# Performance work log

Hardware: AMD Instinct MI355X
Metric: run time of the kernel (lower is better)

## Reference

```python
import jax, jax.numpy as jnp
import numpy as np

N_NODES = 50000
N_EDGES = 800000
DIM = 64
N_REL = 16
N_Q = 8192
FEAT = 4
N_LAYERS = 2


def setup_inputs() -> dict:
    key = jax.random.key(0)
    ks = jax.random.split(key, 16)
    s = 0.1
    return {
        "node_feat": jax.random.normal(ks[0], (N_NODES, FEAT), jnp.float32),
        "edge_index": jax.random.randint(ks[1], (2, N_EDGES), 0, N_NODES),
        "edge_type": jax.random.randint(ks[2], (N_EDGES,), 0, N_REL),
        "heads": jax.random.randint(ks[3], (N_Q,), 0, N_NODES),
        "rels": jax.random.randint(ks[4], (N_Q,), 0, N_REL),
        "tails": jax.random.randint(ks[5], (N_Q,), 0, N_NODES),
        # parameters (stored as [in, out] so y = x @ W + b)
        "in_w": jax.random.normal(ks[6], (FEAT, DIM), jnp.float32) * s,
        "in_b": jnp.zeros((DIM,), jnp.float32),
        "rel_w": jax.random.normal(ks[7], (N_LAYERS, N_REL, DIM, DIM), jnp.float32) * s,
        "self_w": jax.random.normal(ks[8], (N_LAYERS, DIM, DIM), jnp.float32) * s,
        "self_b": jnp.zeros((N_LAYERS, DIM), jnp.float32),
        "rel_emb": jax.random.normal(ks[9], (N_REL, DIM), jnp.float32) * s,
        "sc_w1": jax.random.normal(ks[10], (3 * DIM, DIM), jnp.float32) * s,
        "sc_b1": jnp.zeros((DIM,), jnp.float32),
        "sc_w2": jax.random.normal(ks[11], (DIM, 1), jnp.float32) * s,
        "sc_b2": jnp.zeros((1,), jnp.float32),
    }


def reference(node_feat, edge_index, edge_type, heads, rels, tails,
              in_w, in_b, rel_w, self_w, self_b, rel_emb,
              sc_w1, sc_b1, sc_w2, sc_b2):
    N = node_feat.shape[0]
    src, dst = edge_index[0], edge_index[1]
    # encoder input projection
    x = jax.nn.relu(node_feat @ in_w + in_b)  # [N, D]
    # degree normalization (same deg for every layer)
    deg = jax.ops.segment_sum(jnp.ones_like(dst, dtype=x.dtype), dst, num_segments=N)
    deg = jnp.maximum(deg, 1.0)[:, None]  # [N, 1]
    L = rel_w.shape[0]
    for l in range(L):
        out = x @ self_w[l] + self_b[l]  # self-loop, [N, D]
        # per-relation transform of every node, then per-edge gather by (src, rel)
        # equals the torch per-relation masked gather->matmul->scatter_add
        xw = jnp.einsum('nd,rdo->nro', x, rel_w[l])  # [N, R, D]
        msg = xw[src, edge_type]                     # [E, D]
        agg = jax.ops.segment_sum(msg, dst, num_segments=N)  # [N, D]
        x = jax.nn.relu(out + agg / deg)
    # scoring
    z_h = x[heads]
    z_t = x[tails]
    r = rel_emb[rels]
    c = jnp.concatenate([z_h, z_t, r], axis=-1)  # [Q, 3D]
    h = jax.nn.relu(c @ sc_w1 + sc_b1)
    return (h @ sc_w2 + sc_b2)[:, 0]  # [Q]
```

## Files before the change

kernel.cpp:

```cpp
#include <hip/hip_runtime.h>
#include <hip/hip_bf16.h>
#include <cstdint>
#include <cstddef>

#define N_NODES 50000
#define N_EDGES 800000
#define DIM 64
#define N_REL 16
#define N_Q 8192
#define NKEY (N_NODES * 16)
#define KDIM 1088
#define SROW 1096
#define TILE 16
#define NKB 34
#define WTL (4 * NKB * 512)
#define NBKT 196

#define NB_PROJ 12500
#define NB_WPREP 544
#define NB_BINA 196
#define NB_W1P 48
#define NB_REB 4

typedef __attribute__((ext_vector_type(8))) short bf16x8;
typedef __attribute__((ext_vector_type(4))) float f32x4;

__device__ __forceinline__ unsigned short f2bf(float f) {
    unsigned int b = __float_as_uint(f);
    return (unsigned short)((b + 0x7FFFu + ((b >> 16) & 1u)) >> 16);
}
__device__ __forceinline__ float bf2f(unsigned short u) {
    return __uint_as_float(((unsigned int)u) << 16);
}

__global__ __launch_bounds__(256) void k_prep(
    const float* __restrict__ nf, const float* __restrict__ inw,
    const float* __restrict__ inb, unsigned short* __restrict__ xbf,
    const float* __restrict__ rel_w, const float* __restrict__ self_w,
    unsigned short* __restrict__ wt, const int* __restrict__ dst,
    int* __restrict__ btot, const float* __restrict__ sc_w1,
    unsigned short* __restrict__ w1p, const float* __restrict__ rel_emb,
    unsigned short* __restrict__ reb)
{
    __shared__ int h[NBKT];
    const int b = blockIdx.x, tid = threadIdx.x;
    if (b < NB_PROJ) {
        int t = b * 256 + tid;
        int n = t >> 6, o = t & 63;
        float4 f = *reinterpret_cast<const float4*>(nf + (size_t)n * 4);
        float a = inb[o] + f.x * inw[o] + f.y * inw[64 + o] + f.z * inw[128 + o] + f.w * inw[192 + o];
        xbf[t] = f2bf(a > 0.f ? a : 0.f);
    } else if (b < NB_PROJ + NB_WPREP) {
        int i = (b - NB_PROJ) * 256 + tid;
        int j = i & 7;
        int lane = (i >> 3) & 63;
        int rest = i >> 9;
        int t = rest % NKB;
        int gl = rest / NKB;
        int g = gl & 3;
        int l = gl >> 2;
        int col = g * 16 + (lane & 15);
        int k = t * 32 + (lane >> 4) * 8 + j;
        float v;
        if (k < 1024) {
            int r = k >> 6, d = k & 63;
            v = rel_w[(((size_t)l * 16 + r) * 64 + d) * 64 + col];
        } else {
            int d = k - 1024;
            v = self_w[((size_t)l * 64 + d) * 64 + col];
        }
        wt[i] = f2bf(v);
    } else if (b < NB_PROJ + NB_WPREP + NB_BINA) {
        const int t = tid;
        if (t < NBKT) h[t] = 0;
        __syncthreads();
        const int e0 = (b - NB_PROJ - NB_WPREP) * 4096;
        #pragma unroll
        for (int j = 0; j < 16; ++j) {
            int e = e0 + j * 256 + t;
            if (e < N_EDGES) atomicAdd(&h[dst[e] >> 8], 1);
        }
        __syncthreads();
        if (t < NBKT && h[t]) atomicAdd(&btot[t], h[t]);
    } else if (b < NB_PROJ + NB_WPREP + NB_BINA + NB_W1P) {
        int i = (b - NB_PROJ - NB_WPREP - NB_BINA) * 256 + tid;
        int j = i & 7;
        int lane = (i >> 3) & 63;
        int rest = i >> 9;
        int t = rest % 6;
        int g = rest / 6;
        int col = g * 16 + (lane & 15);
        int k = t * 32 + (lane >> 4) * 8 + j;
        w1p[i] = f2bf(sc_w1[k * 64 + col]);
    } else {
        int i = (b - NB_PROJ - NB_WPREP - NB_BINA - NB_W1P) * 256 + tid;
        if (i < N_REL * 64) reb[i] = f2bf(rel_emb[i]);
    }
}

__global__ __launch_bounds__(256) void k_binS(
    const int* __restrict__ btot, int* __restrict__ bbase, int* __restrict__ gcur)
{
    const int t = threadIdx.x;
    int v = (t < NBKT) ? btot[t] : 0;
    const int lane = t & 63, wid = t >> 6;
    int incl = v;
    #pragma unroll
    for (int o = 1; o < 64; o <<= 1) { int u = __shfl_up(incl, o); if (lane >= o) incl += u; }
    __shared__ int ws[4];
    if (lane == 63) ws[wid] = incl;
    __syncthreads();
    int wb = 0;
    #pragma unroll
    for (int w = 0; w < 4; ++w) if (w < wid) wb += ws[w];
    int excl = wb + incl - v;
    if (t < NBKT) { bbase[t] = excl; gcur[t] = excl; }
    if (t == NBKT - 1) bbase[NBKT] = excl + v;
}

__global__ __launch_bounds__(256) void k_binB(
    const int* __restrict__ src, const int* __restrict__ dst, const int* __restrict__ et,
    int* __restrict__ gcur, unsigned int* __restrict__ scratch)
{
    __shared__ int cnt[NBKT], base[NBKT], lcur[NBKT];
    const int t = threadIdx.x;
    if (t < NBKT) cnt[t] = 0;
    __syncthreads();
    const int e0 = blockIdx.x * 4096;
    int dv[16];
    #pragma unroll
    for (int j = 0; j < 16; ++j) {
        int e = e0 + j * 256 + t;
        dv[j] = (e < N_EDGES) ? dst[e] : -1;
        if (dv[j] >= 0) atomicAdd(&cnt[dv[j] >> 8], 1);
    }
    __syncthreads();
    if (t < NBKT) {
        base[t] = cnt[t] ? atomicAdd(&gcur[t], cnt[t]) : 0;
        lcur[t] = 0;
    }
    __syncthreads();
    #pragma unroll
    for (int j = 0; j < 16; ++j) {
        int e = e0 + j * 256 + t;
        if (dv[j] >= 0) {
            int b = dv[j] >> 8;
            int pos = base[b] + atomicAdd(&lcur[b], 1);
            unsigned p = ((unsigned)src[e] << 12) | ((unsigned)(dv[j] & 255) << 4) | (unsigned)et[e];
            scratch[pos] = p;
        }
    }
}

__global__ __launch_bounds__(1024) void k_key2(
    const int* __restrict__ bbase, const unsigned int* __restrict__ scratch,
    int* __restrict__ offs, unsigned int* __restrict__ csr)
{
    __shared__ int hist[4096];
    __shared__ int wsum[16];
    const int t = threadIdx.x;
    const int b = blockIdx.x;
    const int k0 = b * 4096;
    #pragma unroll
    for (int j = 0; j < 4; ++j) hist[t + j * 1024] = 0;
    __syncthreads();
    const int E0 = bbase[b], E1 = bbase[b + 1];
    for (int e = E0 + t; e < E1; e += 1024)
        atomicAdd(&hist[scratch[e] & 0xFFFu], 1);
    __syncthreads();
    int4 h4 = *reinterpret_cast<int4*>(&hist[t * 4]);
    int run = h4.x + h4.y + h4.z + h4.w;
    const int lane = t & 63, wid = t >> 6;
    int incl = run;
    #pragma unroll
    for (int o = 1; o < 64; o <<= 1) { int u = __shfl_up(incl, o); if (lane >= o) incl += u; }
    if (lane == 63) wsum[wid] = incl;
    __syncthreads();
    if (wid == 0) {
        int wv = (lane < 16) ? wsum[lane] : 0;
        #pragma unroll
        for (int o = 1; o < 16; o <<= 1) { int u = __shfl_up(wv, o); if (lane >= o) wv += u; }
        if (lane < 16) wsum[lane] = wv;
    }
    __syncthreads();
    int texcl = (wid ? wsum[wid - 1] : 0) + incl - run;
    int4 cur;
    cur.x = E0 + texcl;
    cur.y = cur.x + h4.x;
    cur.z = cur.y + h4.y;
    cur.w = cur.z + h4.z;
    *reinterpret_cast<int4*>(&hist[t * 4]) = cur;
    if (k0 + t * 4 < NKEY)
        *reinterpret_cast<int4*>(&offs[k0 + t * 4]) = cur;
    if (b == NBKT - 1 && t == 0) offs[NKEY] = N_EDGES;
    __syncthreads();
    for (int e = E0 + t; e < E1; e += 1024) {
        unsigned p = scratch[e];
        int pos = atomicAdd(&hist[p & 0xFFFu], 1);
        csr[pos] = ((p >> 12) << 7) | (p & 15u);
    }
}

__global__ __launch_bounds__(512, 8) void k_layer(
    const unsigned short* __restrict__ xbf_in,
    const int* __restrict__ offs,
    const unsigned int* __restrict__ csr,
    const unsigned short* __restrict__ wt,
    const float* __restrict__ selfb,
    unsigned short* __restrict__ xbf_out)
{
    alignas(16) __shared__ unsigned short S[TILE * SROW];
    const int tid = threadIdx.x, lane = tid & 63;
    const int wid = __builtin_amdgcn_readfirstlane(tid >> 6);
    const int nb = blockIdx.x * TILE;

    #pragma unroll
    for (int s = 0; s < 2; ++s) {
        unsigned int* Sr = reinterpret_cast<unsigned int*>(&S[(wid * 2 + s) * SROW]);
        #pragma unroll
        for (int i = 0; i < 8; ++i) Sr[lane + i * 64] = 0u;
        if (lane < 32) Sr[512 + lane] = 0u;
    }

    #pragma unroll 1
    for (int s = 0; s < 2; ++s) {
        const int nl = wid * 2 + s;
        const int node = nb + nl;
        const int A = offs[node * 16];
        const int B = offs[node * 16 + 16];
        S[nl * SROW + 1024 + lane] = xbf_in[(size_t)node * 64 + lane];
        const int deg = B - A;
        if (deg <= 0) continue;
        const float inv = 1.0f / (float)(deg > 1 ? deg : 1);

        const unsigned loff = (unsigned)(lane << 1);
        unsigned c0[8], c1[8];
        float x0[8], x1[8];
        int cur = -1;
        float acc = 0.f;

        auto loadb = [&](unsigned (&cv)[8], float (&xv)[8], int eb) {
            #pragma unroll
            for (int j = 0; j < 8; ++j) {
                int idx = eb + j;
                idx = idx < B - 1 ? idx : B - 1;
                cv[j] = csr[idx];
            }
            #pragma unroll
            for (int j = 0; j < 8; ++j) {
                unsigned off = (cv[j] & 0xFFFFFF80u) | loff;
                xv[j] = bf2f(*reinterpret_cast<const unsigned short*>(
                    reinterpret_cast<const char*>(xbf_in) + off));
            }
        };
        auto accum = [&](unsigned (&cv)[8], float (&xv)[8], int m) {
            #pragma unroll
            for (int j = 0; j < 8; ++j) {
                if (j < m) {
                    int rj = (int)(cv[j] & 15u);
                    if (rj != cur) {
                        if (cur >= 0) S[nl * SROW + cur * 64 + lane] = f2bf(acc * inv);
                        cur = rj;
                        acc = 0.f;
                    }
                    acc += xv[j];
                }
            }
        };

        int e0 = A;
        int m0 = deg > 8 ? 8 : deg;
        loadb(c0, x0, e0);
        for (;;) {
            int e1 = e0 + 8;
            int m1 = B - e1;
            m1 = m1 > 8 ? 8 : m1;
            if (m1 > 0) loadb(c1, x1, e1);
            accum(c0, x0, m0);
            if (m1 <= 0) break;
            int e2 = e1 + 8;
            m0 = B - e2;
            m0 = m0 > 8 ? 8 : m0;
            if (m0 > 0) loadb(c0, x0, e2);
            accum(c1, x1, m1);
            if (m0 <= 0) break;
            e0 = e2;
        }
        if (cur >= 0) S[nl * SROW + cur * 64 + lane] = f2bf(acc * inv);
    }
    __syncthreads();

    const int g = wid & 3, kh = wid >> 2;
    const int t0 = kh * 17;
    const int colg = lane & 15, kg = lane >> 4;
    f32x4 acc0 = {0.f, 0.f, 0.f, 0.f};
    const unsigned short* wb = wt + (size_t)g * (NKB * 512) + (size_t)lane * 8 + (size_t)t0 * 512;
    const unsigned short* sa0 = &S[colg * SROW + kg * 8 + t0 * 32];
    #pragma unroll 1
    for (int t = 0; t < 17; ++t) {
        bf16x8 b  = *reinterpret_cast<const bf16x8*>(wb + (size_t)t * 512);
        bf16x8 a0 = *reinterpret_cast<const bf16x8*>(sa0 + t * 32);
        acc0 = __builtin_amdgcn_mfma_f32_16x16x32_bf16(a0, b, acc0, 0, 0, 0);
    }
    __syncthreads();
    float4* scr = reinterpret_cast<float4*>(S);
    if (kh == 1) {
        scr[g * 64 + lane] = make_float4(acc0[0], acc0[1], acc0[2], acc0[3]);
    }
    __syncthreads();
    if (kh == 0) {
        float4 q0 = scr[g * 64 + lane];
        acc0[0] += q0.x; acc0[1] += q0.y; acc0[2] += q0.z; acc0[3] += q0.w;
        const int col = g * 16 + colg;
        const float sb = selfb[col];
        #pragma unroll
        for (int j = 0; j < 4; ++j) {
            int n0 = nb + kg * 4 + j;
            float v0 = acc0[j] + sb;
            v0 = v0 > 0.f ? v0 : 0.f;
            xbf_out[(size_t)n0 * 64 + col] = f2bf(v0);
        }
    }
}

__global__ __launch_bounds__(256) void k_score(
    const unsigned short* __restrict__ x, const int* __restrict__ heads,
    const int* __restrict__ rels, const int* __restrict__ tails,
    const unsigned short* __restrict__ reb, const unsigned short* __restrict__ w1p,
    const float* __restrict__ b1, const float* __restrict__ w2,
    const float* __restrict__ b2, float* __restrict__ out)
{
    __shared__ float scr[64];
    const int tid = threadIdx.x, lane = tid & 63, w = tid >> 6;
    const int qbase = blockIdx.x * 16;
    const int ql = lane & 15, kg = lane >> 4;
    const int q = qbase + ql;
    const unsigned short* zh = x + (size_t)heads[q] * 64 + kg * 8;
    const unsigned short* zt = x + (size_t)tails[q] * 64 + kg * 8;
    const unsigned short* re = reb + rels[q] * 64 + kg * 8;
    bf16x8 a0 = *reinterpret_cast<const bf16x8*>(zh);
    bf16x8 a1 = *reinterpret_cast<const bf16x8*>(zh + 32);
    bf16x8 a2 = *reinterpret_cast<const bf16x8*>(zt);
    bf16x8 a3 = *reinterpret_cast<const bf16x8*>(zt + 32);
    bf16x8 a4 = *reinterpret_cast<const bf16x8*>(re);
    bf16x8 a5 = *reinterpret_cast<const bf16x8*>(re + 32);
    const unsigned short* wb = w1p + (size_t)w * (6 * 512) + (size_t)lane * 8;
    f32x4 acc = {0.f, 0.f, 0.f, 0.f};
    acc = __builtin_amdgcn_mfma_f32_16x16x32_bf16(a0, *reinterpret_cast<const bf16x8*>(wb + 0 * 512), acc, 0, 0, 0);
    acc = __builtin_amdgcn_mfma_f32_16x16x32_bf16(a1, *reinterpret_cast<const bf16x8*>(wb + 1 * 512), acc, 0, 0, 0);
    acc = __builtin_amdgcn_mfma_f32_16x16x32_bf16(a2, *reinterpret_cast<const bf16x8*>(wb + 2 * 512), acc, 0, 0, 0);
    acc = __builtin_amdgcn_mfma_f32_16x16x32_bf16(a3, *reinterpret_cast<const bf16x8*>(wb + 3 * 512), acc, 0, 0, 0);
    acc = __builtin_amdgcn_mfma_f32_16x16x32_bf16(a4, *reinterpret_cast<const bf16x8*>(wb + 4 * 512), acc, 0, 0, 0);
    acc = __builtin_amdgcn_mfma_f32_16x16x32_bf16(a5, *reinterpret_cast<const bf16x8*>(wb + 5 * 512), acc, 0, 0, 0);
    const int col = w * 16 + ql;
    const float b1c = b1[col], w2c = w2[col];
    float p[4];
    #pragma unroll
    for (int j = 0; j < 4; ++j) {
        float hh = acc[j] + b1c;
        hh = hh > 0.f ? hh : 0.f;
        p[j] = hh * w2c;
    }
    #pragma unroll
    for (int o = 1; o < 16; o <<= 1) {
        p[0] += __shfl_xor(p[0], o);
        p[1] += __shfl_xor(p[1], o);
        p[2] += __shfl_xor(p[2], o);
        p[3] += __shfl_xor(p[3], o);
    }
    if (ql == 0) {
        #pragma unroll
        for (int j = 0; j < 4; ++j) scr[w * 16 + kg * 4 + j] = p[j];
    }
    __syncthreads();
    if (tid < 16)
        out[qbase + tid] = scr[tid] + scr[16 + tid] + scr[32 + tid] + scr[48 + tid] + b2[0];
}

extern "C" void kernel_launch(void* const* d_in, const int* in_sizes, int n_in,
                              void* d_out, int out_size, void* d_ws, size_t ws_size,
                              hipStream_t stream)
{
    const float* node_feat = (const float*)d_in[0];
    const int* edge_index  = (const int*)d_in[1];
    const int* edge_type   = (const int*)d_in[2];
    const int* heads       = (const int*)d_in[3];
    const int* rels        = (const int*)d_in[4];
    const int* tails       = (const int*)d_in[5];
    const float* in_w      = (const float*)d_in[6];
    const float* in_b      = (const float*)d_in[7];
    const float* rel_w     = (const float*)d_in[8];
    const float* self_w    = (const float*)d_in[9];
    const float* self_b    = (const float*)d_in[10];
    const float* rel_emb   = (const float*)d_in[11];
    const float* sc_w1     = (const float*)d_in[12];
    const float* sc_b1     = (const float*)d_in[13];
    const float* sc_w2     = (const float*)d_in[14];
    const float* sc_b2     = (const float*)d_in[15];
    float* out = (float*)d_out;

    char* ws = (char*)d_ws;
    size_t off = 0;
    auto alloc = [&](size_t bytes) -> void* {
        void* p = ws + off;
        off = (off + bytes + 255) & ~(size_t)255;
        return p;
    };
    unsigned short* xbf_a = (unsigned short*)alloc((size_t)N_NODES * 64 * 2);
    unsigned short* xbf_b = (unsigned short*)alloc((size_t)N_NODES * 64 * 2);
    int* offs             = (int*)alloc((size_t)(NKEY + 1) * 4);
    unsigned int* scratch = (unsigned int*)alloc((size_t)N_EDGES * 4);
    unsigned int* csr     = (unsigned int*)alloc((size_t)N_EDGES * 4);
    unsigned short* wt    = (unsigned short*)alloc((size_t)2 * WTL * 2);
    unsigned short* w1p   = (unsigned short*)alloc((size_t)4 * 6 * 512 * 2);
    unsigned short* reb   = (unsigned short*)alloc((size_t)N_REL * 64 * 2);
    int* btot             = (int*)alloc(NBKT * 4);
    int* bbase            = (int*)alloc((NBKT + 1) * 4);
    int* gcur             = (int*)alloc(NBKT * 4);

    const int* src = edge_index;
    const int* dst = edge_index + N_EDGES;

    hipMemsetAsync(btot, 0, NBKT * 4, stream);
    k_prep<<<NB_PROJ + NB_WPREP + NB_BINA + NB_W1P + NB_REB, 256, 0, stream>>>(
        node_feat, in_w, in_b, xbf_a, rel_w, self_w, wt, dst, btot,
        sc_w1, w1p, rel_emb, reb);
    k_binS<<<1, 256, 0, stream>>>(btot, bbase, gcur);
    k_binB<<<(N_EDGES + 4095) / 4096, 256, 0, stream>>>(src, dst, edge_type, gcur, scratch);
    k_key2<<<NBKT, 1024, 0, stream>>>(bbase, scratch, offs, csr);

    for (int l = 0; l < 2; ++l) {
        const unsigned short* xin = (l == 0) ? xbf_a : xbf_b;
        unsigned short* xout = (l == 0) ? xbf_b : xbf_a;
        k_layer<<<N_NODES / TILE, 512, 0, stream>>>(
            xin, offs, csr, wt + (size_t)l * WTL, self_b + l * 64, xout);
    }
    k_score<<<N_Q / 16, 256, 0, stream>>>(xbf_a, heads, rels, tails, reb, w1p,
                                          sc_b1, sc_w2, sc_b2, out);
}
```

Baseline: 141.7 us.

## Balance edge aggregation across waves by splitting the tile's CSR range evenly

Instead of each wave handling two fixed nodes (which leaves waves idle when degrees differ), the tile's whole contiguous CSR edge range is split evenly across the 8 waves. Each split boundary is moved forward to the next (node, relation) key change so no segment is shared between waves. The node index within the tile is packed into the top bits of each CSR entry. Degree normalization is moved out of the aggregation and applied after the MFMA: the self-loop K-blocks go into a separate accumulator so only the relation part is scaled by 1/deg. The cost is extra boundary-scan loads and a second accumulator reduced through shared memory.

```diff
diff --git a/kernel.cpp b/kernel.cpp
--- a/kernel.cpp
+++ b/kernel.cpp
@@ -197,7 +197,7 @@
     for (int e = E0 + t; e < E1; e += 1024) {
         unsigned p = scratch[e];
         int pos = atomicAdd(&hist[p & 0xFFFu], 1);
-        csr[pos] = ((p >> 12) << 7) | (p & 15u);
+        csr[pos] = (((p >> 4) & 15u) << 28) | ((p >> 12) << 7) | (p & 15u);
     }
 }
 
@@ -210,113 +210,163 @@
     unsigned short* __restrict__ xbf_out)
 {
     alignas(16) __shared__ unsigned short S[TILE * SROW];
+    __shared__ float invs[TILE];
     const int tid = threadIdx.x, lane = tid & 63;
     const int wid = __builtin_amdgcn_readfirstlane(tid >> 6);
     const int nb = blockIdx.x * TILE;
 
     #pragma unroll
     for (int s = 0; s < 2; ++s) {
-        unsigned int* Sr = reinterpret_cast<unsigned int*>(&S[(wid * 2 + s) * SROW]);
+        const int nl = wid * 2 + s;
+        unsigned int* Sr = reinterpret_cast<unsigned int*>(&S[nl * SROW]);
         #pragma unroll
         for (int i = 0; i < 8; ++i) Sr[lane + i * 64] = 0u;
-        if (lane < 32) Sr[512 + lane] = 0u;
-    }
-
-    #pragma unroll 1
-    for (int s = 0; s < 2; ++s) {
-        const int nl = wid * 2 + s;
         const int node = nb + nl;
-        const int A = offs[node * 16];
-        const int B = offs[node * 16 + 16];
         S[nl * SROW + 1024 + lane] = xbf_in[(size_t)node * 64 + lane];
-        const int deg = B - A;
-        if (deg <= 0) continue;
-        const float inv = 1.0f / (float)(deg > 1 ? deg : 1);
-
-        const unsigned loff = (unsigned)(lane << 1);
-        unsigned c0[8], c1[8];
-        float x0[8], x1[8];
-        int cur = -1;
-        float acc = 0.f;
-
-        auto loadb = [&](unsigned (&cv)[8], float (&xv)[8], int eb) {
-            #pragma unroll
-            for (int j = 0; j < 8; ++j) {
-                int idx = eb + j;
-                idx = idx < B - 1 ? idx : B - 1;
-                cv[j] = csr[idx];
-            }
-            #pragma unroll
-            for (int j = 0; j < 8; ++j) {
-                unsigned off = (cv[j] & 0xFFFFFF80u) | loff;
-                xv[j] = bf2f(*reinterpret_cast<const unsigned short*>(
-                    reinterpret_cast<const char*>(xbf_in) + off));
-            }
-        };
-        auto accum = [&](unsigned (&cv)[8], float (&xv)[8], int m) {
-            #pragma unroll
-            for (int j = 0; j < 8; ++j) {
-                if (j < m) {
-                    int rj = (int)(cv[j] & 15u);
-                    if (rj != cur) {
-                        if (cur >= 0) S[nl * SROW + cur * 64 + lane] = f2bf(acc * inv);
-                        cur = rj;
-                        acc = 0.f;
-                    }
-                    acc += xv[j];
+        if (lane == 0) {
+            int dg = offs[node * 16 + 16] - offs[node * 16];
+            invs[nl] = 1.0f / (float)(dg > 1 ? dg : 1);
+        }
+    }
+    const int E0 = offs[nb * 16];
+    const int E1 = offs[(nb + TILE) * 16];
+    __syncthreads();
+
+    {
+        const int total = E1 - E0;
+        const int per = (total + 7) >> 3;
+        int i = E0 + wid * per;
+        int we = i + per; we = we < E1 ? we : E1;
+        int myEnd = we;
+        if (i >= E1) { i = E1; myEnd = E1; }
+        else {
+            if (wid > 0) {
+                unsigned pv = csr[i - 1];
+                unsigned kp = ((pv >> 28) << 4) | (pv & 15u);
+                while (i < we) {
+                    unsigned cc = csr[i];
+                    if ((((cc >> 28) << 4) | (cc & 15u)) != kp) break;
+                    ++i;
                 }
             }
-        };
-
-        int e0 = A;
-        int m0 = deg > 8 ? 8 : deg;
-        loadb(c0, x0, e0);
-        for (;;) {
-            int e1 = e0 + 8;
-            int m1 = B - e1;
-            m1 = m1 > 8 ? 8 : m1;
-            if (m1 > 0) loadb(c1, x1, e1);
-            accum(c0, x0, m0);
-            if (m1 <= 0) break;
-            int e2 = e1 + 8;
-            m0 = B - e2;
-            m0 = m0 > 8 ? 8 : m0;
-            if (m0 > 0) loadb(c0, x0, e2);
-            accum(c1, x1, m1);
-            if (m0 <= 0) break;
-            e0 = e2;
-        }
-        if (cur >= 0) S[nl * SROW + cur * 64 + lane] = f2bf(acc * inv);
+            if (myEnd < E1 && myEnd > i) {
+                unsigned lv = csr[myEnd - 1];
+                unsigned kl = ((lv >> 28) << 4) | (lv & 15u);
+                while (myEnd < E1) {
+                    unsigned cc = csr[myEnd];
+                    if ((((cc >> 28) << 4) | (cc & 15u)) != kl) break;
+                    ++myEnd;
+                }
+            }
+        }
+        const int deg = myEnd - i;
+        if (deg > 0) {
+            const unsigned loff = (unsigned)(lane << 1);
+            unsigned c0[8], c1[8];
+            float x0[8], x1[8];
+            int cur = -1;
+            float acc = 0.f;
+
+            auto loadb = [&](unsigned (&cv)[8], float (&xv)[8], int eb) {
+                #pragma unroll
+                for (int j = 0; j < 8; ++j) {
+                    int idx = eb + j;
+                    idx = idx < myEnd - 1 ? idx : myEnd - 1;
+                    cv[j] = csr[idx];
+                }
+                #pragma unroll
+                for (int j = 0; j < 8; ++j) {
+                    unsigned off = (cv[j] & 0x0FFFFF80u) | loff;
+                    xv[j] = bf2f(*reinterpret_cast<const unsigned short*>(
+                        reinterpret_cast<const char*>(xbf_in) + off));
+                }
+            };
+            auto accum = [&](unsigned (&cv)[8], float (&xv)[8], int m) {
+                #pragma unroll
+                for (int j = 0; j < 8; ++j) {
+                    if (j < m) {
+                        int kj = (int)(((cv[j] >> 28) << 4) | (cv[j] & 15u));
+                        if (kj != cur) {
+                            if (cur >= 0) S[(cur >> 4) * SROW + (cur & 15) * 64 + lane] = f2bf(acc);
+                            cur = kj;
+                            acc = 0.f;
+                        }
+                        acc += xv[j];
+                    }
+                }
+            };
+
+            int e0 = i;
+            int m0 = deg > 8 ? 8 : deg;
+            loadb(c0, x0, e0);
+            for (;;) {
+                int e1 = e0 + 8;
+                int m1 = myEnd - e1;
+                m1 = m1 > 8 ? 8 : m1;
+                if (m1 > 0) loadb(c1, x1, e1);
+                accum(c0, x0, m0);
+                if (m1 <= 0) break;
+                int e2 = e1 + 8;
+                m0 = myEnd - e2;
+                m0 = m0 > 8 ? 8 : m0;
+                if (m0 > 0) loadb(c0, x0, e2);
+                accum(c1, x1, m1);
+                if (m0 <= 0) break;
+                e0 = e2;
+            }
+            if (cur >= 0) S[(cur >> 4) * SROW + (cur & 15) * 64 + lane] = f2bf(acc);
+        }
     }
     __syncthreads();
 
     const int g = wid & 3, kh = wid >> 2;
     const int t0 = kh * 17;
     const int colg = lane & 15, kg = lane >> 4;
-    f32x4 acc0 = {0.f, 0.f, 0.f, 0.f};
+    f32x4 accR = {0.f, 0.f, 0.f, 0.f};
+    f32x4 accS = {0.f, 0.f, 0.f, 0.f};
     const unsigned short* wb = wt + (size_t)g * (NKB * 512) + (size_t)lane * 8 + (size_t)t0 * 512;
     const unsigned short* sa0 = &S[colg * SROW + kg * 8 + t0 * 32];
-    #pragma unroll 1
-    for (int t = 0; t < 17; ++t) {
-        bf16x8 b  = *reinterpret_cast<const bf16x8*>(wb + (size_t)t * 512);
-        bf16x8 a0 = *reinterpret_cast<const bf16x8*>(sa0 + t * 32);
-        acc0 = __builtin_amdgcn_mfma_f32_16x16x32_bf16(a0, b, acc0, 0, 0, 0);
+    if (kh == 0) {
+        #pragma unroll 1
+        for (int t = 0; t < 17; ++t) {
+            bf16x8 b  = *reinterpret_cast<const bf16x8*>(wb + (size_t)t * 512);
+            bf16x8 a0 = *reinterpret_cast<const bf16x8*>(sa0 + t * 32);
+            accR = __builtin_amdgcn_mfma_f32_16x16x32_bf16(a0, b, accR, 0, 0, 0);
+        }
+    } else {
+        #pragma unroll 1
+        for (int t = 0; t < 15; ++t) {
+            bf16x8 b  = *reinterpret_cast<const bf16x8*>(wb + (size_t)t * 512);
+            bf16x8 a0 = *reinterpret_cast<const bf16x8*>(sa0 + t * 32);
+            accR = __builtin_amdgcn_mfma_f32_16x16x32_bf16(a0, b, accR, 0, 0, 0);
+        }
+        #pragma unroll
+        for (int t = 15; t < 17; ++t) {
+            bf16x8 b  = *reinterpret_cast<const bf16x8*>(wb + (size_t)t * 512);
+            bf16x8 a0 = *reinterpret_cast<const bf16x8*>(sa0 + t * 32);
+            accS = __builtin_amdgcn_mfma_f32_16x16x32_bf16(a0, b, accS, 0, 0, 0);
+        }
     }
     __syncthreads();
     float4* scr = reinterpret_cast<float4*>(S);
     if (kh == 1) {
-        scr[g * 64 + lane] = make_float4(acc0[0], acc0[1], acc0[2], acc0[3]);
+        scr[g * 64 + lane]       = make_float4(accR[0], accR[1], accR[2], accR[3]);
+        scr[256 + g * 64 + lane] = make_float4(accS[0], accS[1], accS[2], accS[3]);
     }
     __syncthreads();
     if (kh == 0) {
-        float4 q0 = scr[g * 64 + lane];
-        acc0[0] += q0.x; acc0[1] += q0.y; acc0[2] += q0.z; acc0[3] += q0.w;
+        float4 qR = scr[g * 64 + lane];
+        float4 qS = scr[256 + g * 64 + lane];
+        accR[0] += qR.x; accR[1] += qR.y; accR[2] += qR.z; accR[3] += qR.w;
+        accS[0] += qS.x; accS[1] += qS.y; accS[2] += qS.z; accS[3] += qS.w;
+        const float4 iv4 = *reinterpret_cast<const float4*>(&invs[kg * 4]);
+        const float iv[4] = {iv4.x, iv4.y, iv4.z, iv4.w};
         const int col = g * 16 + colg;
         const float sb = selfb[col];
         #pragma unroll
         for (int j = 0; j < 4; ++j) {
             int n0 = nb + kg * 4 + j;
-            float v0 = acc0[j] + sb;
+            float v0 = accR[j] * iv[j] + accS[j] + sb;
             v0 = v0 > 0.f ? v0 : 0.f;
             xbf_out[(size_t)n0 * 64 + col] = f2bf(v0);
         }
```

New measurement: 153.0 us. +8.0%, slower.
